# Kernel tuning notes

Hardware: AMD Instinct MI355X
Metric: run time of the kernel (lower is better)

The kernel has to match this reference:

```python
import jax, jax.numpy as jnp
import numpy as np

EPS = 1e-8  # torch.cosine_similarity norm clamp

def setup_inputs() -> dict:
    key = jax.random.key(0)
    k1, k2, k3, k4 = jax.random.split(key, 4)
    B, S, D, C = 64, 512, 768, 512
    V = jax.random.normal(k1, (B, S, D), dtype=jnp.float32)
    label_embeddings = jax.random.normal(k2, (C, D), dtype=jnp.float32)
    fc_w = jax.random.normal(k3, (C, D), dtype=jnp.float32) * 0.02
    fc_b = jax.random.normal(k4, (C,), dtype=jnp.float32) * 0.02
    return {"V": V, "label_embeddings": label_embeddings, "fc_w": fc_w, "fc_b": fc_b}

def reference(V, label_embeddings, fc_w, fc_b):
    # Normalized embeddings (cosine similarity = dot of unit vectors, norms clamped at EPS)
    Vn = V / jnp.maximum(jnp.linalg.norm(V, axis=-1, keepdims=True), EPS)
    Ln = label_embeddings / jnp.maximum(
        jnp.linalg.norm(label_embeddings, axis=-1, keepdims=True), EPS)
    # [B, S, C] cosine similarities, then max over classes -> per-token weight m [B, S]
    sims = jnp.einsum('bsd,cd->bsc', Vn, Ln)
    m = jnp.max(sims, axis=-1)
    # Softmax over sequence dim -> attention beta [B, S]
    beta = jax.nn.softmax(m, axis=-1)
    # Weighted sum of token embeddings: z = V^T beta  -> [B, D]
    z = jnp.einsum('bsd,bs->bd', V, beta)
    # Final classifier
    out = z @ fc_w.T + fc_b
    return (out, z)
```

## Files before the change

kernel.cpp:

```cpp
#include <hip/hip_runtime.h>
#include <cstdint>
#include <cstddef>

#define BB 64
#define SS 512
#define DD 768
#define CC 512

typedef __attribute__((ext_vector_type(8))) short short8;
typedef __attribute__((ext_vector_type(4))) float f32x4;

#define GLOBAL_AS __attribute__((address_space(1)))
#define LDS_AS __attribute__((address_space(3)))

static __device__ __forceinline__ unsigned short f2bf(float f) {
  union { float f; unsigned u; } v; v.f = f;
  unsigned u = v.u;
  u += 0x7FFFu + ((u >> 16) & 1u);
  return (unsigned short)(u >> 16);
}

static __device__ __forceinline__ void async_copy16(const void* g, void* l) {
  __builtin_amdgcn_global_load_lds((const GLOBAL_AS void*)g, (LDS_AS void*)l,
                                   16, 0, 0);
}

__global__ __launch_bounds__(256) void k_label_norm(const float* __restrict__ L,
                                                    unsigned short* __restrict__ Lnb) {
  const int c = blockIdx.x;
  const int tid = threadIdx.x;
  const float* row = L + (size_t)c * DD;
  float v[3];
  float s = 0.f;
#pragma unroll
  for (int k = 0; k < 3; k++) { v[k] = row[tid + 256 * k]; s += v[k] * v[k]; }
#pragma unroll
  for (int o = 32; o > 0; o >>= 1) s += __shfl_xor(s, o, 64);
  __shared__ float wsum[4];
  if ((tid & 63) == 0) wsum[tid >> 6] = s;
  __syncthreads();
  const float tot = wsum[0] + wsum[1] + wsum[2] + wsum[3];
  const float inv = 1.f / fmaxf(sqrtf(tot), 1e-8f);
  unsigned short* ochunk = Lnb + (size_t)(c >> 4) * (16 * DD);
  const int mr = c & 15;
#pragma unroll
  for (int k = 0; k < 3; k++) {
    const int d = tid + 256 * k;
    const int kc = d >> 5;
    const int q = (d >> 3) & 3;
    const int j = d & 7;
    ochunk[kc * 512 + q * 128 + mr * 8 + j] = f2bf(v[k] * inv);
  }
}

__global__ __launch_bounds__(256) void k_sims_max(const float* __restrict__ V,
                                                  const unsigned short* __restrict__ Lnb,
                                                  float* __restrict__ m_out) {
  const int tid = threadIdx.x;
  const int wave = tid >> 6;
  const int lane = tid & 63;
  const int q = lane >> 4;
  const int mr = lane & 15;
  const int64_t tokBase = (int64_t)blockIdx.x * 64 + wave * 16;

  __shared__ unsigned short Bs[2][16 * DD];
  __shared__ float nrmS[4][16];

  {
    const char* src = (const char*)Lnb;
    char* dst = (char*)&Bs[0][0];
#pragma unroll
    for (int i = wave; i < 24; i += 4)
      async_copy16(src + i * 1024 + lane * 16, dst + i * 1024);
  }

  const float* arow = V + (tokBase + mr) * DD + q * 8;
  short8 afrag[24];
  float nrm2 = 0.f;
#pragma unroll
  for (int kc = 0; kc < 24; kc++) {
    const float4* p = (const float4*)(arow + kc * 32);
    const float4 x = p[0];
    const float4 y = p[1];
    short8 a;
    a[0] = (short)f2bf(x.x); a[1] = (short)f2bf(x.y);
    a[2] = (short)f2bf(x.z); a[3] = (short)f2bf(x.w);
    a[4] = (short)f2bf(y.x); a[5] = (short)f2bf(y.y);
    a[6] = (short)f2bf(y.z); a[7] = (short)f2bf(y.w);
    afrag[kc] = a;
    nrm2 += x.x * x.x + x.y * x.y + x.z * x.z + x.w * x.w;
    nrm2 += y.x * y.x + y.y * y.y + y.z * y.z + y.w * y.w;
  }
  nrm2 += __shfl_xor(nrm2, 16, 64);
  nrm2 += __shfl_xor(nrm2, 32, 64);
  if (q == 0) nrmS[wave][mr] = nrm2;

  __syncthreads();

  const int laneByte = lane * 16;
  f32x4 vmax = {-3e38f, -3e38f, -3e38f, -3e38f};
  for (int cc = 0; cc < 32; cc++) {
    const int p = cc & 1;
    if (cc + 1 < 32) {
      const char* src = (const char*)(Lnb + (size_t)(cc + 1) * 16 * DD);
      char* dst = (char*)&Bs[p ^ 1][0];
#pragma unroll
      for (int i = wave; i < 24; i += 4)
        async_copy16(src + i * 1024 + lane * 16, dst + i * 1024);
    }
    f32x4 acc = {0.f, 0.f, 0.f, 0.f};
    const char* bbase = (const char*)&Bs[p][0] + laneByte;
    short8 bf[4];
#pragma unroll
    for (int j = 0; j < 4; j++) bf[j] = *(const short8*)(bbase + j * 1024);
#pragma unroll
    for (int kc = 0; kc < 24; kc++) {
      acc = __builtin_amdgcn_mfma_f32_16x16x32_bf16(afrag[kc], bf[kc & 3], acc, 0, 0, 0);
      if (kc + 4 < 24) bf[kc & 3] = *(const short8*)(bbase + (kc + 4) * 1024);
    }
    vmax[0] = fmaxf(vmax[0], acc[0]);
    vmax[1] = fmaxf(vmax[1], acc[1]);
    vmax[2] = fmaxf(vmax[2], acc[2]);
    vmax[3] = fmaxf(vmax[3], acc[3]);
    __syncthreads();
  }
#pragma unroll
  for (int o = 1; o < 16; o <<= 1) {
#pragma unroll
    for (int r = 0; r < 4; r++) vmax[r] = fmaxf(vmax[r], __shfl_xor(vmax[r], o, 64));
  }
  if (mr == 0) {
#pragma unroll
    for (int r = 0; r < 4; r++) {
      const float nr = nrmS[wave][q * 4 + r];
      m_out[tokBase + q * 4 + r] = vmax[r] / fmaxf(sqrtf(nr), 1e-8f);
    }
  }
}

__global__ __launch_bounds__(256) void k_softmax(const float* __restrict__ m,
                                                 float* __restrict__ beta) {
  const int b = blockIdx.x;
  const int tid = threadIdx.x;
  const float* mb = m + (size_t)b * SS;
  const float v0 = mb[tid];
  const float v1 = mb[tid + 256];
  float mx = fmaxf(v0, v1);
#pragma unroll
  for (int o = 32; o > 0; o >>= 1) mx = fmaxf(mx, __shfl_xor(mx, o, 64));
  __shared__ float wred[4];
  if ((tid & 63) == 0) wred[tid >> 6] = mx;
  __syncthreads();
  mx = fmaxf(fmaxf(wred[0], wred[1]), fmaxf(wred[2], wred[3]));
  const float e0 = __expf(v0 - mx);
  const float e1 = __expf(v1 - mx);
  float s = e0 + e1;
#pragma unroll
  for (int o = 32; o > 0; o >>= 1) s += __shfl_xor(s, o, 64);
  __syncthreads();
  if ((tid & 63) == 0) wred[tid >> 6] = s;
  __syncthreads();
  s = wred[0] + wred[1] + wred[2] + wred[3];
  const float inv = 1.f / s;
  float* bb = beta + (size_t)b * SS;
  bb[tid] = e0 * inv;
  bb[tid + 256] = e1 * inv;
}

__global__ __launch_bounds__(192) void k_zpart(const float* __restrict__ V,
                                               const float* __restrict__ beta,
                                               float* __restrict__ zpart,
                                               int spc, int nsc) {
  const int blk = blockIdx.x;
  const int b = blk / nsc;
  const int sc = blk % nsc;
  const int tid = threadIdx.x;
  const float* vb = V + ((size_t)b * SS + (size_t)sc * spc) * DD + tid * 4;
  const float* bb = beta + (size_t)b * SS + (size_t)sc * spc;
  float4 acc = {0.f, 0.f, 0.f, 0.f};
#pragma unroll 4
  for (int s = 0; s < spc; s++) {
    const float w = bb[s];
    const float4 x = *(const float4*)(vb + (size_t)s * DD);
    acc.x += w * x.x; acc.y += w * x.y; acc.z += w * x.z; acc.w += w * x.w;
  }
  *(float4*)(zpart + (size_t)blk * DD + tid * 4) = acc;
}

__global__ __launch_bounds__(256) void k_final(const float* __restrict__ zpart,
                                               const float* __restrict__ fc_w,
                                               const float* __restrict__ fc_b,
                                               float* __restrict__ out,
                                               float* __restrict__ zout,
                                               int nsc) {
  const int b = blockIdx.x >> 1;
  const int half = blockIdx.x & 1;
  const int tid = threadIdx.x;
  __shared__ float zs[DD];
  for (int i = tid; i < DD; i += 256) {
    float s = 0.f;
    for (int sc = 0; sc < nsc; sc++) s += zpart[((size_t)b * nsc + sc) * DD + i];
    zs[i] = s;
    if (half == 0) zout[(size_t)b * DD + i] = s;
  }
  __syncthreads();
  const int c = half * 256 + tid;
  const float4* w = (const float4*)(fc_w + (size_t)c * DD);
  float acc = 0.f;
  for (int d4 = 0; d4 < DD / 4; d4++) {
    const float4 ww = w[d4];
    acc += ww.x * zs[d4 * 4] + ww.y * zs[d4 * 4 + 1] +
           ww.z * zs[d4 * 4 + 2] + ww.w * zs[d4 * 4 + 3];
  }
  out[(size_t)b * CC + c] = acc + fc_b[c];
}

extern "C" void kernel_launch(void* const* d_in, const int* in_sizes, int n_in,
                              void* d_out, int out_size, void* d_ws, size_t ws_size,
                              hipStream_t stream) {
  const float* V  = (const float*)d_in[0];
  const float* L  = (const float*)d_in[1];
  const float* fw = (const float*)d_in[2];
  const float* fb = (const float*)d_in[3];
  float* out = (float*)d_out;

  char* ws = (char*)d_ws;
  unsigned short* Lnb = (unsigned short*)ws;
  float* m     = (float*)(ws + 786432);
  float* beta  = (float*)(ws + 917504);
  float* zpart = (float*)(ws + 1048576);

  const int nsc = (ws_size >= (size_t)1048576 + (size_t)16 * BB * DD * 4) ? 16 : 8;
  const int spc = SS / nsc;

  k_label_norm<<<CC, 256, 0, stream>>>(L, Lnb);
  k_sims_max<<<512, 256, 0, stream>>>(V, Lnb, m);
  k_softmax<<<BB, 256, 0, stream>>>(m, beta);
  k_zpart<<<BB * nsc, 192, 0, stream>>>(V, beta, zpart, spc, nsc);
  k_final<<<2 * BB, 256, 0, stream>>>(zpart, fw, fb, out, out + BB * CC, nsc);
}
```

Measured before the change: 241.2 us.

## Triple-buffer label chunks with partial vmcnt waits and per-block chunk rotation

The sims-max kernel moves from double to triple buffering of the normalized label chunks in LDS. It prefetches two chunks ahead and waits only on the older loads with s_waitcnt vmcnt(6) instead of a full __syncthreads drain. Each block also starts at a chunk offset set by its block index, so concurrent blocks read different label chunks and spread L2 traffic. This costs 24KB more LDS per block, which may reduce occupancy, and relies on hand-counted outstanding-load numbers being correct.

```diff
diff --git a/kernel.cpp b/kernel.cpp
--- a/kernel.cpp
+++ b/kernel.cpp
@@ -62,17 +62,22 @@
   const int q = lane >> 4;
   const int mr = lane & 15;
   const int64_t tokBase = (int64_t)blockIdx.x * 64 + wave * 16;
-
-  __shared__ unsigned short Bs[2][16 * DD];
+  const int rot = blockIdx.x & 31;
+
+  __shared__ unsigned short Bs[3][16 * DD];
   __shared__ float nrmS[4][16];
 
-  {
-    const char* src = (const char*)Lnb;
-    char* dst = (char*)&Bs[0][0];
-#pragma unroll
-    for (int i = wave; i < 24; i += 4)
-      async_copy16(src + i * 1024 + lane * 16, dst + i * 1024);
-  }
+#define STAGE_CHUNK(chunk, bufidx)                                        \
+  {                                                                       \
+    const char* src_ = (const char*)(Lnb + (size_t)(chunk) * 16 * DD);    \
+    char* dst_ = (char*)&Bs[bufidx][0];                                   \
+    _Pragma("unroll")                                                     \
+    for (int i_ = wave; i_ < 24; i_ += 4)                                 \
+      async_copy16(src_ + i_ * 1024 + lane * 16, dst_ + i_ * 1024);       \
+  }
+
+  STAGE_CHUNK(rot, 0);
+  STAGE_CHUNK((rot + 1) & 31, 1);
 
   const float* arow = V + (tokBase + mr) * DD + q * 8;
   short8 afrag[24];
@@ -99,17 +104,13 @@
 
   const int laneByte = lane * 16;
   f32x4 vmax = {-3e38f, -3e38f, -3e38f, -3e38f};
+  int bi = 0;
+  int bs = 2;
   for (int cc = 0; cc < 32; cc++) {
-    const int p = cc & 1;
-    if (cc + 1 < 32) {
-      const char* src = (const char*)(Lnb + (size_t)(cc + 1) * 16 * DD);
-      char* dst = (char*)&Bs[p ^ 1][0];
-#pragma unroll
-      for (int i = wave; i < 24; i += 4)
-        async_copy16(src + i * 1024 + lane * 16, dst + i * 1024);
-    }
+    if (cc + 2 < 32) STAGE_CHUNK((cc + 2 + rot) & 31, bs);
+
     f32x4 acc = {0.f, 0.f, 0.f, 0.f};
-    const char* bbase = (const char*)&Bs[p][0] + laneByte;
+    const char* bbase = (const char*)&Bs[bi][0] + laneByte;
     short8 bf[4];
 #pragma unroll
     for (int j = 0; j < 4; j++) bf[j] = *(const short8*)(bbase + j * 1024);
@@ -122,8 +123,21 @@
     vmax[1] = fmaxf(vmax[1], acc[1]);
     vmax[2] = fmaxf(vmax[2], acc[2]);
     vmax[3] = fmaxf(vmax[3], acc[3]);
-    __syncthreads();
-  }
+
+    if (cc < 31) {
+      if (cc + 2 < 32) {
+        asm volatile("s_waitcnt vmcnt(6)" ::: "memory");
+      } else {
+        asm volatile("s_waitcnt vmcnt(0)" ::: "memory");
+      }
+      __builtin_amdgcn_s_barrier();
+      __builtin_amdgcn_sched_barrier(0);
+    }
+    bi = (bi == 2) ? 0 : bi + 1;
+    bs = (bs == 2) ? 0 : bs + 1;
+  }
+#undef STAGE_CHUNK
+
 #pragma unroll
   for (int o = 1; o < 16; o <<= 1) {
 #pragma unroll
```

New measurement: 266.3 us. +10.4%, slower.
